# Kernel tuning notes

Measured on AMD Instinct MI355X. Metric: run time of the kernel, lower is better.

## Reference

```python
import jax, jax.numpy as jnp
import numpy as np

C = 16          # cardinality (hard-coded in GraphHead)
E = 1024        # node_encoding_size == representation_size (residual requires equality)
S = 1024        # spatial_head output size (hard-coded Linear(256,1024))
R = 1024        # representation_size
D = R // C      # sub_repr_size = 64
NS, NO = 64, 256
NUM_ITER = 2
EPS = 1e-5


def _w(key, shape, fan_in):
    return jax.random.normal(key, shape, dtype=jnp.float32) * np.float32((2.0 / fan_in) ** 0.5)


def setup_inputs() -> dict:
    key = jax.random.key(0)
    ks = jax.random.split(key, 16)
    inp = {
        'h': jax.random.normal(ks[0], (NS, E), dtype=jnp.float32),
        'o': jax.random.normal(ks[1], (NO, E), dtype=jnp.float32),
        'spatial': jax.random.normal(ks[2], (NS, NO, S), dtype=jnp.float32),
        # attention_head: MultiBranchFusion(2E, 1024, R, 16)
        'att_w1': _w(ks[3], (C, 2 * E, D), 2 * E), 'att_b1': jnp.zeros((C, D), jnp.float32),
        'att_w2': _w(ks[4], (C, S, D), S),         'att_b2': jnp.zeros((C, D), jnp.float32),
        'att_w3': _w(ks[5], (C, D, R), D),         'att_b3': jnp.zeros((C, R), jnp.float32),
        # sub_to_obj: MessageMBF(E, 1024, R, 'subject', 16)
        's2o_w1': _w(ks[6], (C, E, D), E),         's2o_b1': jnp.zeros((C, D), jnp.float32),
        's2o_w2': _w(ks[7], (C, S, D), S),         's2o_b2': jnp.zeros((C, D), jnp.float32),
        's2o_w3': _w(ks[8], (C, D, R), D),         's2o_b3': jnp.zeros((C, R), jnp.float32),
        # obj_to_sub: MessageMBF(E, 1024, R, 'object', 16)
        'o2s_w1': _w(ks[9], (C, E, D), E),         'o2s_b1': jnp.zeros((C, D), jnp.float32),
        'o2s_w2': _w(ks[10], (C, S, D), S),        'o2s_b2': jnp.zeros((C, D), jnp.float32),
        'o2s_w3': _w(ks[11], (C, D, R), D),        'o2s_b3': jnp.zeros((C, R), jnp.float32),
        # adjacency: Linear(R, 1)
        'adj_w': _w(ks[12], (R, 1), R), 'adj_b': jnp.zeros((1,), jnp.float32),
        # LayerNorms
        'ns_g': jnp.ones((E,), jnp.float32), 'ns_b': jnp.zeros((E,), jnp.float32),
        'no_g': jnp.ones((E,), jnp.float32), 'no_b': jnp.zeros((E,), jnp.float32),
    }
    return inp


def _layernorm(x, g, b):
    m = jnp.mean(x, axis=-1, keepdims=True)
    v = jnp.mean((x - m) ** 2, axis=-1, keepdims=True)
    return (x - m) * jax.lax.rsqrt(v + EPS) * g + b


def _mbf_pair(app, spa, w1, b1, w2, b2, w3, b3):
    # app [ns,no,A], spa [ns,no,S] -> [ns,no,R]; sum over C branches of fc3(relu(fc1*fc2))
    a = jnp.einsum('ija,cad->cijd', app, w1) + b1[:, None, None, :]
    s = jnp.einsum('ijs,csd->cijd', spa, w2) + b2[:, None, None, :]
    g = jax.nn.relu(a * s)
    return jnp.einsum('cijd,cdr->ijr', g, w3) + b3.sum(0)


def _msg_subject(h, spa, w1, b1, w2, b2, w3, b3):
    # MessageMBF subject: broadcast fc1(h) [ns,d] against fc2(spa) [ns,no,d]
    a = jnp.einsum('ia,cad->cid', h, w1) + b1[:, None, :]
    s = jnp.einsum('ijs,csd->cijd', spa, w2) + b2[:, None, None, :]
    g = jax.nn.relu(a[:, :, None, :] * s)
    return jnp.einsum('cijd,cdr->ijr', g, w3) + b3.sum(0)  # [ns,no,R]


def _msg_object(o, spa, w1, b1, w2, b2, w3, b3):
    # MessageMBF object: broadcast fc1(o) [no,d] against fc2(spa) [ns,no,d]
    a = jnp.einsum('ja,cad->cjd', o, w1) + b1[:, None, :]
    s = jnp.einsum('ijs,csd->cijd', spa, w2) + b2[:, None, None, :]
    g = jax.nn.relu(a[:, None, :, :] * s)
    return jnp.einsum('cijd,cdr->ijr', g, w3) + b3.sum(0)  # [ns,no,R]


def reference(h, o, spatial,
              att_w1, att_b1, att_w2, att_b2, att_w3, att_b3,
              s2o_w1, s2o_b1, s2o_w2, s2o_b2, s2o_w3, s2o_b3,
              o2s_w1, o2s_b1, o2s_w2, o2s_b2, o2s_w3, o2s_b3,
              adj_w, adj_b, ns_g, ns_b, no_g, no_b):
    ns, no = h.shape[0], o.shape[0]
    for _ in range(NUM_ITER):
        # edge weights via attention MBF on concatenated pair encodings
        pair_app = jnp.concatenate([
            jnp.broadcast_to(h[:, None, :], (ns, no, E)),
            jnp.broadcast_to(o[None, :, :], (ns, no, E)),
        ], axis=-1)
        w = jax.nn.relu(_mbf_pair(pair_app, spatial, att_w1, att_b1, att_w2, att_b2, att_w3, att_b3))
        adj = jnp.einsum('ijr,rk->ij', w, adj_w) + adj_b[0]  # [ns,no]
        # update subject nodes from object messages
        m_o2s = _msg_object(o, spatial, o2s_w1, o2s_b1, o2s_w2, o2s_b2, o2s_w3, o2s_b3)
        msg_h = jax.nn.relu(jnp.einsum('ij,ijr->ir', jax.nn.softmax(adj, axis=1), m_o2s))
        h = _layernorm(h + msg_h, ns_g, ns_b)
        # update object nodes from (updated) subject messages
        m_s2o = _msg_subject(h, spatial, s2o_w1, s2o_b1, s2o_w2, s2o_b2, s2o_w3, s2o_b3)
        msg_o = jax.nn.relu(jnp.einsum('ij,ijr->jr', jax.nn.softmax(adj, axis=0), m_s2o))
        o = _layernorm(o + msg_o, no_g, no_b)
    return jnp.concatenate([h, o], axis=0)  # [ns+no, E]
```

## Files before the change

### kernel.cpp

```cpp
#include <hip/hip_runtime.h>
#include <cstdint>
#include <cstddef>

typedef _Float16 hf;
typedef _Float16 h8v __attribute__((ext_vector_type(8)));
typedef float f4v __attribute__((ext_vector_type(4)));

#define NS 64
#define NO 256
#define MP 16384
#define KD 1024

__device__ __forceinline__ h8v cvt8(float4 a, float4 b) {
    h8v r;
    r[0] = (hf)a.x; r[1] = (hf)a.y; r[2] = (hf)a.z; r[3] = (hf)a.w;
    r[4] = (hf)b.x; r[5] = (hf)b.y; r[6] = (hf)b.z; r[7] = (hf)b.w;
    return r;
}
__device__ __forceinline__ float f4at(const float4& a, const float4& b, int e) {
    const float* p = e < 4 ? (const float*)&a : (const float*)&b;
    return p[e & 3];
}
__device__ __forceinline__ void gl16(const hf* g, hf* l) {
    __builtin_amdgcn_global_load_lds(
        (const __attribute__((address_space(1))) void*)g,
        (__attribute__((address_space(3))) void*)l, 16, 0, 0);
}

__global__ void k_pack16(const float* __restrict__ src, hf* __restrict__ dst, int n8) {
    int g = blockIdx.x * 256 + threadIdx.x;
    if (g >= n8) return;
    const float4* s4 = (const float4*)src;
    float4 a = s4[2 * g], b = s4[2 * g + 1];
    *(h8v*)(dst + (size_t)g * 8) = cvt8(a, b);
}

struct RoR { const float* src; hf* dhi; hf* dlo; int Asrc; int aOff; };
struct RoRs { RoR r[7]; };
__global__ void k_reorder16b(RoRs RR) {
    const RoR rt = RR.r[blockIdx.z];
    __shared__ float tile[64][65];
    int c = blockIdx.x, a0 = blockIdx.y * 64;
    int t = threadIdx.x, lx = t & 63, ly = t >> 6;
#pragma unroll
    for (int p = 0; p < 16; ++p) {
        int ar = ly + p * 4;
        tile[ar][lx] = rt.src[(size_t)(c * rt.Asrc + rt.aOff + a0 + ar) * 64 + lx];
    }
    __syncthreads();
#pragma unroll
    for (int p = 0; p < 16; ++p) {
        int d = ly + p * 4;
        float v = tile[lx][d];
        hf h = (hf)v;
        size_t idx = (size_t)(c * 64 + d) * 1024 + a0 + lx;
        rt.dhi[idx] = h;
        if (rt.dlo) rt.dlo[idx] = (hf)(v - (float)h);
    }
}

struct TrR { const float* src; hf* dhi; hf* dlo; };
struct TrRs { TrR r[3]; };
__global__ void k_transpose16b(TrRs RR) {
    const TrR rt = RR.r[blockIdx.z];
    __shared__ float tile[64][65];
    int r0 = blockIdx.x * 64, s0 = blockIdx.y * 64;
    int t = threadIdx.x, lx = t & 63, ly = t >> 6;
#pragma unroll
    for (int p = 0; p < 16; ++p) {
        int srow = ly + p * 4;
        tile[srow][lx] = rt.src[(size_t)(s0 + srow) * 1024 + r0 + lx];
    }
    __syncthreads();
#pragma unroll
    for (int p = 0; p < 16; ++p) {
        int rr = ly + p * 4;
        float v = tile[lx][rr];
        hf h = (hf)v;
        size_t idx = (size_t)(r0 + rr) * 1024 + s0 + lx;
        rt.dhi[idx] = h;
        if (rt.dlo) rt.dlo[idx] = (hf)(v - (float)h);
    }
}

__global__ void k_prep_bc(const float* __restrict__ ab2, const float* __restrict__ ob2,
                          const float* __restrict__ sb2, const float* __restrict__ ab3,
                          const float* __restrict__ ob3, const float* __restrict__ sb3,
                          float* __restrict__ b2cat, float* __restrict__ b3a,
                          float* __restrict__ b3o, float* __restrict__ b3s) {
    int g = blockIdx.x * 256 + threadIdx.x;
    if (g >= 1024) return;
    b2cat[g] = ab2[g]; b2cat[1024 + g] = ob2[g]; b2cat[2048 + g] = sb2[g];
    float sa = 0.f, so = 0.f, ss = 0.f;
    for (int c = 0; c < 16; ++c) {
        sa += ab3[c * 1024 + g];
        so += ob3[c * 1024 + g];
        ss += sb3[c * 1024 + g];
    }
    b3a[g] = sa; b3o[g] = so; b3s[g] = ss;
}

__global__ void k_init_ho(const float* __restrict__ h, const float* __restrict__ o,
                          float* __restrict__ outbuf, hf* __restrict__ h16, hf* __restrict__ o16) {
    int g = blockIdx.x * 256 + threadIdx.x;
    if (g < NS * KD) { float v = h[g]; outbuf[g] = v; h16[g] = (hf)v; }
    int g2 = g - NS * KD;
    if (g2 >= 0 && g2 < NO * KD) { float v = o[g2]; outbuf[NS * KD + g2] = v; o16[g2] = (hf)v; }
}

__global__ __launch_bounds__(256, 2) void k_prep_gemm(
    const hf* __restrict__ sp16,
    const hf* __restrict__ Wah, const hf* __restrict__ Wal,
    const hf* __restrict__ Wo2, const hf* __restrict__ Ws2,
    const float* __restrict__ b2cat,
    hf* __restrict__ Sh, hf* __restrict__ Sl,
    hf* __restrict__ So, hf* __restrict__ Ss) {
    __shared__ hf Ah[4096];
    __shared__ hf Bh[8192];
    __shared__ hf Bl[8192];
    const int tid = threadIdx.x;
    int lin = blockIdx.y * 12 + blockIdx.x;
    int xcd = lin & 7, slot = lin >> 3;
    int xn = slot % 12;
    const int m0 = ((xcd << 4) + slot / 12) * 128;
    const int plane = xn >> 2;
    const int nbase = (xn & 3) * 256;
    const hf* Bb = plane == 0 ? Wah : (plane == 1 ? Wo2 : Ws2);
    const bool hasL = (plane == 0);
    const int lane = tid & 63, wid = tid >> 6;
    const int wm = wid >> 1, wn = wid & 1;
    const int lr = lane & 15, lg = lane >> 4;
    const int rsl = (lg ^ ((lr >> 1) & 3)) * 8;

    const int crow = lane >> 2;
    const int gseg = ((lane & 3) ^ ((lane >> 3) & 3)) * 8;
    hf* ldsA0 = Ah + wid * 512;
    hf* ldsA1 = Ah + 2048 + wid * 512;
    hf* ldsB0 = Bh + wid * 512;         hf* ldsB1 = Bh + 2048 + wid * 512;
    hf* ldsB2 = Bh + 4096 + wid * 512;  hf* ldsB3 = Bh + 6144 + wid * 512;
    hf* ldsL0 = Bl + wid * 512;         hf* ldsL1 = Bl + 2048 + wid * 512;
    hf* ldsL2 = Bl + 4096 + wid * 512;  hf* ldsL3 = Bl + 6144 + wid * 512;
    const hf* gA0 = sp16 + (size_t)(m0 + wid * 16 + crow) * KD + gseg;
    const hf* gA1 = sp16 + (size_t)(m0 + 64 + wid * 16 + crow) * KD + gseg;
    const hf* gB0 = Bb  + (size_t)(nbase +       wid * 16 + crow) * KD + gseg;
    const hf* gB1 = Bb  + (size_t)(nbase + 64  + wid * 16 + crow) * KD + gseg;
    const hf* gB2 = Bb  + (size_t)(nbase + 128 + wid * 16 + crow) * KD + gseg;
    const hf* gB3 = Bb  + (size_t)(nbase + 192 + wid * 16 + crow) * KD + gseg;
    const hf* gL0 = Wal + (size_t)(nbase +       wid * 16 + crow) * KD + gseg;
    const hf* gL1 = Wal + (size_t)(nbase + 64  + wid * 16 + crow) * KD + gseg;
    const hf* gL2 = Wal + (size_t)(nbase + 128 + wid * 16 + crow) * KD + gseg;
    const hf* gL3 = Wal + (size_t)(nbase + 192 + wid * 16 + crow) * KD + gseg;

    f4v acc[2][4][4];
    f4v zz; zz[0] = 0.f; zz[1] = 0.f; zz[2] = 0.f; zz[3] = 0.f;
#pragma unroll
    for (int u = 0; u < 2; ++u)
#pragma unroll
        for (int a = 0; a < 4; ++a)
#pragma unroll
            for (int b = 0; b < 4; ++b) acc[u][a][b] = zz;

    for (int t = 0; t < 32; ++t) {
        const int kk = t * 32;
        __syncthreads();
        gl16(gA0 + kk, ldsA0);
        gl16(gA1 + kk, ldsA1);
        gl16(gB0 + kk, ldsB0); gl16(gB1 + kk, ldsB1);
        gl16(gB2 + kk, ldsB2); gl16(gB3 + kk, ldsB3);
        if (hasL) {
            gl16(gL0 + kk, ldsL0); gl16(gL1 + kk, ldsL1);
            gl16(gL2 + kk, ldsL2); gl16(gL3 + kk, ldsL3);
        }
        __syncthreads();
        h8v fa[4], fb[4];
#pragma unroll
        for (int x = 0; x < 4; ++x)
            fa[x] = *(const h8v*)(Ah + (wm * 64 + x * 16 + lr) * 32 + rsl);
#pragma unroll
        for (int u = 0; u < 2; ++u) {
#pragma unroll
            for (int x = 0; x < 4; ++x)
                fb[x] = *(const h8v*)(Bh + u * 4096 + (wn * 64 + x * 16 + lr) * 32 + rsl);
#pragma unroll
            for (int mi = 0; mi < 4; ++mi)
#pragma unroll
                for (int ni = 0; ni < 4; ++ni)
                    acc[u][mi][ni] = __builtin_amdgcn_mfma_f32_16x16x32_f16(fa[mi], fb[ni], acc[u][mi][ni], 0, 0, 0);
            if (hasL) {
#pragma unroll
                for (int x = 0; x < 4; ++x)
                    fb[x] = *(const h8v*)(Bl + u * 4096 + (wn * 64 + x * 16 + lr) * 32 + rsl);
#pragma unroll
                for (int mi = 0; mi < 4; ++mi)
#pragma unroll
                    for (int ni = 0; ni < 4; ++ni)
                        acc[u][mi][ni] = __builtin_amdgcn_mfma_f32_16x16x32_f16(fa[mi], fb[ni], acc[u][mi][ni], 0, 0, 0);
            }
        }
    }
#pragma unroll
    for (int u = 0; u < 2; ++u)
#pragma unroll
        for (int mi = 0; mi < 4; ++mi)
#pragma unroll
            for (int ni = 0; ni < 4; ++ni)
#pragma unroll
                for (int r = 0; r < 4; ++r) {
                    int gr = m0 + wm * 64 + mi * 16 + lg * 4 + r;
                    int col = nbase + u * 128 + wn * 64 + ni * 16 + lr;
                    float v = acc[u][mi][ni][r] + b2cat[plane * 1024 + col];
                    size_t idx = (size_t)gr * KD + col;
                    if (plane == 0) {
                        hf hi = (hf)v;
                        Sh[idx] = hi; Sl[idx] = (hf)(v - (float)hi);
                    } else if (plane == 1) So[idx] = (hf)v;
                    else Ss[idx] = (hf)v;
                }
}

__global__ void k_build_g(const hf* __restrict__ Sh, const hf* __restrict__ Sl,
                          const float* __restrict__ e1, const float* __restrict__ e2,
                          hf* __restrict__ Gh) {
    int g = blockIdx.x * 256 + threadIdx.x;
    size_t base = (size_t)g * 8;
    int m = (int)(base >> 10);
    int k = (int)(base & 1023);
    int i = m >> 8, j = m & 255;
    h8v sh = *(const h8v*)(Sh + base);
    h8v sl = *(const h8v*)(Sl + base);
    float4 ex0 = *(const float4*)(e1 + (size_t)i * KD + k);
    float4 ex1 = *(const float4*)(e1 + (size_t)i * KD + k + 4);
    float4 ey0 = *(const float4*)(e2 + (size_t)j * KD + k);
    float4 ey1 = *(const float4*)(e2 + (size_t)j * KD + k + 4);
    h8v gh;
#pragma unroll
    for (int e = 0; e < 8; ++e) {
        float s = (float)sh[e] + (float)sl[e];
        float ee = f4at(ex0, ex1, e) + f4at(ey0, ey1, e);
        float gg = ee * s; gg = gg > 0.f ? gg : 0.f;
        gh[e] = (hf)gg;
    }
    *(h8v*)(Gh + base) = gh;
}

__global__ __launch_bounds__(256, 2) void k_adj_gemm(
    const hf* __restrict__ Gh, const hf* __restrict__ W3h, const hf* __restrict__ W3l,
    const float* __restrict__ b3, const float* __restrict__ aw,
    float* __restrict__ adjv) {
    __shared__ hf Ah[4096];
    __shared__ hf Bh[8192];
    __shared__ hf Bl[8192];
    const int tid = threadIdx.x;
    int lin = blockIdx.y * 4 + blockIdx.x;
    int xcd = lin & 7, slot = lin >> 3;
    const int nbase = (slot & 3) * 256;
    const int m0 = ((xcd << 4) + (slot >> 2)) * 128;
    const int lane = tid & 63, wid = tid >> 6;
    const int wm = wid >> 1, wn = wid & 1;
    const int lr = lane & 15, lg = lane >> 4;
    const int srow = tid >> 2, sseg = tid & 3;
    const int wo_ = srow * 32 + (sseg ^ ((srow >> 1) & 3)) * 8;
    const int rsl = (lg ^ ((lr >> 1) & 3)) * 8;
    const int ar0 = m0 + srow, ar1 = ar0 + 64;
    const int ko = sseg * 8;

    f4v acc[2][4][4];
    f4v zz; zz[0] = 0.f; zz[1] = 0.f; zz[2] = 0.f; zz[3] = 0.f;
#pragma unroll
    for (int u = 0; u < 2; ++u)
#pragma unroll
        for (int a = 0; a < 4; ++a)
#pragma unroll
            for (int b = 0; b < 4; ++b) acc[u][a][b] = zz;

    h8v va0, va1, vb00, vb01, vb10, vb11, wb00, wb01, wb10, wb11;
    auto LOAD = [&](int kk) {
        va0 = *(const h8v*)(Gh + (size_t)ar0 * KD + ko + kk);
        va1 = *(const h8v*)(Gh + (size_t)ar1 * KD + ko + kk);
        vb00 = *(const h8v*)(W3h + (size_t)(nbase + srow) * KD + ko + kk);
        vb01 = *(const h8v*)(W3h + (size_t)(nbase + 64 + srow) * KD + ko + kk);
        vb10 = *(const h8v*)(W3h + (size_t)(nbase + 128 + srow) * KD + ko + kk);
        vb11 = *(const h8v*)(W3h + (size_t)(nbase + 192 + srow) * KD + ko + kk);
        wb00 = *(const h8v*)(W3l + (size_t)(nbase + srow) * KD + ko + kk);
        wb01 = *(const h8v*)(W3l + (size_t)(nbase + 64 + srow) * KD + ko + kk);
        wb10 = *(const h8v*)(W3l + (size_t)(nbase + 128 + srow) * KD + ko + kk);
        wb11 = *(const h8v*)(W3l + (size_t)(nbase + 192 + srow) * KD + ko + kk);
    };
    LOAD(0);
    for (int t = 0; t < 32; ++t) {
        __syncthreads();
        *(h8v*)(Ah + wo_) = va0; *(h8v*)(Ah + 2048 + wo_) = va1;
        *(h8v*)(Bh + wo_) = vb00; *(h8v*)(Bh + 2048 + wo_) = vb01;
        *(h8v*)(Bh + 4096 + wo_) = vb10; *(h8v*)(Bh + 6144 + wo_) = vb11;
        *(h8v*)(Bl + wo_) = wb00; *(h8v*)(Bl + 2048 + wo_) = wb01;
        *(h8v*)(Bl + 4096 + wo_) = wb10; *(h8v*)(Bl + 6144 + wo_) = wb11;
        __syncthreads();
        if (t + 1 < 32) LOAD((t + 1) * 32);
        h8v fa[4], fb[4];
#pragma unroll
        for (int x = 0; x < 4; ++x)
            fa[x] = *(const h8v*)(Ah + (wm * 64 + x * 16 + lr) * 32 + rsl);
#pragma unroll
        for (int u = 0; u < 2; ++u) {
#pragma unroll
            for (int x = 0; x < 4; ++x)
                fb[x] = *(const h8v*)(Bh + u * 4096 + (wn * 64 + x * 16 + lr) * 32 + rsl);
#pragma unroll
            for (int mi = 0; mi < 4; ++mi)
#pragma unroll
                for (int ni = 0; ni < 4; ++ni)
                    acc[u][mi][ni] = __builtin_amdgcn_mfma_f32_16x16x32_f16(fa[mi], fb[ni], acc[u][mi][ni], 0, 0, 0);
#pragma unroll
            for (int x = 0; x < 4; ++x)
                fb[x] = *(const h8v*)(Bl + u * 4096 + (wn * 64 + x * 16 + lr) * 32 + rsl);
#pragma unroll
            for (int mi = 0; mi < 4; ++mi)
#pragma unroll
                for (int ni = 0; ni < 4; ++ni)
                    acc[u][mi][ni] = __builtin_amdgcn_mfma_f32_16x16x32_f16(fa[mi], fb[ni], acc[u][mi][ni], 0, 0, 0);
        }
    }
    float b3v[2][4], awv[2][4];
#pragma unroll
    for (int u = 0; u < 2; ++u)
#pragma unroll
        for (int ni = 0; ni < 4; ++ni) {
            int gc = nbase + u * 128 + wn * 64 + ni * 16 + lr;
            b3v[u][ni] = b3[gc]; awv[u][ni] = aw[gc];
        }
#pragma unroll
    for (int mi = 0; mi < 4; ++mi)
#pragma unroll
        for (int r = 0; r < 4; ++r) {
            float part = 0.f;
#pragma unroll
            for (int u = 0; u < 2; ++u)
#pragma unroll
                for (int ni = 0; ni < 4; ++ni) {
                    float w = acc[u][mi][ni][r] + b3v[u][ni];
                    w = w > 0.f ? w : 0.f;
                    part += w * awv[u][ni];
                }
            part += __shfl_xor(part, 1);
            part += __shfl_xor(part, 2);
            part += __shfl_xor(part, 4);
            part += __shfl_xor(part, 8);
            if (lr == 0) atomicAdd(adjv + m0 + wm * 64 + mi * 16 + lg * 4 + r, part);
        }
}

struct SRoute { const hf* A; const hf* Bh; const hf* Bl; float* C; const float* bias; int m0; int M; };
struct SRoutes { SRoute r[5]; };

__global__ __launch_bounds__(256) void k_small(SRoutes RR) {
    const SRoute rt = RR.r[blockIdx.y];
    __shared__ hf Ah[4096];
    __shared__ hf Bh[4096];
    __shared__ hf Bl[4096];
    const int tid = threadIdx.x;
    const int n0 = blockIdx.x * 128;
    const int kbeg = blockIdx.z * 128;
    const int lane = tid & 63, wid = tid >> 6;
    const int wm = wid >> 1, wn = wid & 1;
    const int lr = lane & 15, lg = lane >> 4;
    const int srow = tid >> 2, sseg = tid & 3;
    const int wo_ = srow * 32 + (sseg ^ ((srow >> 1) & 3)) * 8;
    const int rsl = (lg ^ ((lr >> 1) & 3)) * 8;
    int ar0 = rt.m0 + srow;      if (ar0 >= rt.M) ar0 = rt.M - 1;
    int ar1 = rt.m0 + 64 + srow; if (ar1 >= rt.M) ar1 = rt.M - 1;
    const bool hasL = rt.Bl != nullptr;
    const int ko = kbeg + sseg * 8;

    f4v acc[4][4];
    f4v zz; zz[0] = 0.f; zz[1] = 0.f; zz[2] = 0.f; zz[3] = 0.f;
#pragma unroll
    for (int a = 0; a < 4; ++a)
#pragma unroll
        for (int b = 0; b < 4; ++b) acc[a][b] = zz;

    h8v va0, va1, vb0, vb1, wb0, wb1;
    auto LOAD = [&](int kk) {
        va0 = *(const h8v*)(rt.A + (size_t)ar0 * KD + ko + kk);
        va1 = *(const h8v*)(rt.A + (size_t)ar1 * KD + ko + kk);
        vb0 = *(const h8v*)(rt.Bh + (size_t)(n0 + srow) * KD + ko + kk);
        vb1 = *(const h8v*)(rt.Bh + (size_t)(n0 + 64 + srow) * KD + ko + kk);
        if (hasL) {
            wb0 = *(const h8v*)(rt.Bl + (size_t)(n0 + srow) * KD + ko + kk);
            wb1 = *(const h8v*)(rt.Bl + (size_t)(n0 + 64 + srow) * KD + ko + kk);
        }
    };
    LOAD(0);
    for (int t = 0; t < 4; ++t) {
        __syncthreads();
        *(h8v*)(Ah + wo_) = va0; *(h8v*)(Ah + 2048 + wo_) = va1;
        *(h8v*)(Bh + wo_) = vb0; *(h8v*)(Bh + 2048 + wo_) = vb1;
        if (hasL) { *(h8v*)(Bl + wo_) = wb0; *(h8v*)(Bl + 2048 + wo_) = wb1; }
        __syncthreads();
        if (t + 1 < 4) LOAD((t + 1) * 32);
        h8v fa[4], fb[4];
#pragma unroll
        for (int x = 0; x < 4; ++x) {
            fa[x] = *(const h8v*)(Ah + (wm * 64 + x * 16 + lr) * 32 + rsl);
            fb[x] = *(const h8v*)(Bh + (wn * 64 + x * 16 + lr) * 32 + rsl);
        }
#pragma unroll
        for (int mi = 0; mi < 4; ++mi)
#pragma unroll
            for (int ni = 0; ni < 4; ++ni)
                acc[mi][ni] = __builtin_amdgcn_mfma_f32_16x16x32_f16(fa[mi], fb[ni], acc[mi][ni], 0, 0, 0);
        if (hasL) {
#pragma unroll
            for (int x = 0; x < 4; ++x)
                fb[x] = *(const h8v*)(Bl + (wn * 64 + x * 16 + lr) * 32 + rsl);
#pragma unroll
            for (int mi = 0; mi < 4; ++mi)
#pragma unroll
                for (int ni = 0; ni < 4; ++ni)
                    acc[mi][ni] = __builtin_amdgcn_mfma_f32_16x16x32_f16(fa[mi], fb[ni], acc[mi][ni], 0, 0, 0);
        }
    }
#pragma unroll
    for (int mi = 0; mi < 4; ++mi)
#pragma unroll
        for (int ni = 0; ni < 4; ++ni)
#pragma unroll
            for (int r = 0; r < 4; ++r) {
                int gr = rt.m0 + wm * 64 + mi * 16 + lg * 4 + r;
                int gc = n0 + wn * 64 + ni * 16 + lr;
                if (gr < rt.M) {
                    float v = acc[mi][ni][r];
                    if (rt.bias && blockIdx.z == 0) v += rt.bias[gc];
                    atomicAdd(rt.C + (size_t)gr * KD + gc, v);
                }
            }
}

__global__ void k_softmax_both(const float* __restrict__ adj, float* __restrict__ p,
                               float* __restrict__ q) {
    int b = blockIdx.x;
    if (b < NS) {
        __shared__ float red[256];
        int i = b, j = threadIdx.x;
        float x = adj[i * 256 + j];
        red[j] = x; __syncthreads();
        for (int s = 128; s > 0; s >>= 1) { if (j < s) red[j] = fmaxf(red[j], red[j + s]); __syncthreads(); }
        float mx = red[0]; __syncthreads();
        float e = __expf(x - mx);
        red[j] = e; __syncthreads();
        for (int s = 128; s > 0; s >>= 1) { if (j < s) red[j] += red[j + s]; __syncthreads(); }
        p[i * 256 + j] = e / red[0];
    } else {
        int j = (b - NS) * 4 + (threadIdx.x >> 6);
        int i = threadIdx.x & 63;
        float x = adj[i * 256 + j];
        float mx = x;
#pragma unroll
        for (int off = 32; off > 0; off >>= 1) mx = fmaxf(mx, __shfl_xor(mx, off));
        float e = __expf(x - mx);
        float s = e;
#pragma unroll
        for (int off = 32; off > 0; off >>= 1) s += __shfl_xor(s, off);
        q[i * 256 + j] = e / s;
    }
}

__global__ void k_build_Gh(const hf* __restrict__ S, const float* __restrict__ aF,
                           const float* __restrict__ p, hf* __restrict__ Gh) {
    __shared__ float pl[256];
    int i = blockIdx.x;
    int k = blockIdx.y * 256 + threadIdx.x;
    pl[threadIdx.x] = p[i * 256 + threadIdx.x];
    __syncthreads();
    const hf* sp = S + (size_t)(i * 256) * KD + k;
    float acc = 0.f;
#pragma unroll 4
    for (int j = 0; j < 256; ++j) {
        float a = aF[(size_t)j * KD + k];
        float s = (float)sp[(size_t)j * KD];
        float g = a * s; g = g > 0.f ? g : 0.f;
        acc += pl[j] * g;
    }
    Gh[(size_t)i * KD + k] = (hf)acc;
}

__global__ void k_build_Go(const hf* __restrict__ S, const float* __restrict__ aF,
                           const float* __restrict__ q, hf* __restrict__ Go) {
    __shared__ float ql[64];
    int j = blockIdx.x;
    int k = blockIdx.y * 256 + threadIdx.x;
    if (threadIdx.x < 64) ql[threadIdx.x] = q[threadIdx.x * 256 + j];
    __syncthreads();
    const hf* sp = S + (size_t)j * KD + k;
    float acc = 0.f;
#pragma unroll 4
    for (int i = 0; i < 64; ++i) {
        float a = aF[(size_t)i * KD + k];
        float s = (float)sp[(size_t)(i * 256) * KD];
        float g = a * s; g = g > 0.f ? g : 0.f;
        acc += ql[i] * g;
    }
    Go[(size_t)j * KD + k] = (hf)acc;
}

__global__ void k_ln_update(float* __restrict__ x, const float* __restrict__ msg,
                            const float* __restrict__ b3, const float* __restrict__ gamma,
                            const float* __restrict__ beta, hf* __restrict__ x16) {
    __shared__ float red[256];
    int r = blockIdx.x, t = threadIdx.x;
    float v[4];
    float s = 0.f;
#pragma unroll
    for (int e = 0; e < 4; ++e) {
        int idx = t + e * 256;
        float mm = msg[(size_t)r * KD + idx] + b3[idx];
        mm = mm > 0.f ? mm : 0.f;
        v[e] = x[(size_t)r * KD + idx] + mm;
        s += v[e];
    }
    red[t] = s; __syncthreads();
    for (int st = 128; st > 0; st >>= 1) { if (t < st) red[t] += red[t + st]; __syncthreads(); }
    float mean = red[0] * (1.f / 1024.f);
    __syncthreads();
    float s2 = 0.f;
#pragma unroll
    for (int e = 0; e < 4; ++e) { float d = v[e] - mean; s2 += d * d; }
    red[t] = s2; __syncthreads();
    for (int st = 128; st > 0; st >>= 1) { if (t < st) red[t] += red[t + st]; __syncthreads(); }
    float var = red[0] * (1.f / 1024.f);
    float rstd = rsqrtf(var + 1e-5f);
#pragma unroll
    for (int e = 0; e < 4; ++e) {
        int idx = t + e * 256;
        float y = (v[e] - mean) * rstd * gamma[idx] + beta[idx];
        x[(size_t)r * KD + idx] = y;
        x16[(size_t)r * KD + idx] = (hf)y;
    }
}

extern "C" void kernel_launch(void* const* d_in, const int* in_sizes, int n_in,
                              void* d_out, int out_size, void* d_ws, size_t ws_size,
                              hipStream_t stream) {
    const float* h_in    = (const float*)d_in[0];
    const float* o_in    = (const float*)d_in[1];
    const float* spatial = (const float*)d_in[2];
    const float* att_w1  = (const float*)d_in[3];
    const float* att_b1  = (const float*)d_in[4];
    const float* att_w2  = (const float*)d_in[5];
    const float* att_b2  = (const float*)d_in[6];
    const float* att_w3  = (const float*)d_in[7];
    const float* att_b3  = (const float*)d_in[8];
    const float* s2o_w1  = (const float*)d_in[9];
    const float* s2o_b1  = (const float*)d_in[10];
    const float* s2o_w2  = (const float*)d_in[11];
    const float* s2o_b2  = (const float*)d_in[12];
    const float* s2o_w3  = (const float*)d_in[13];
    const float* s2o_b3  = (const float*)d_in[14];
    const float* o2s_w1  = (const float*)d_in[15];
    const float* o2s_b1  = (const float*)d_in[16];
    const float* o2s_w2  = (const float*)d_in[17];
    const float* o2s_b2  = (const float*)d_in[18];
    const float* o2s_w3  = (const float*)d_in[19];
    const float* o2s_b3  = (const float*)d_in[20];
    const float* adj_w   = (const float*)d_in[21];
    const float* ns_g    = (const float*)d_in[23];
    const float* ns_b    = (const float*)d_in[24];
    const float* no_g    = (const float*)d_in[25];
    const float* no_b    = (const float*)d_in[26];

    char* ws = (char*)d_ws;
    size_t off = 0;
    auto alloc = [&](size_t bytes) -> char* {
        char* pp = ws + off;
        off += (bytes + 255) & ~(size_t)255;
        return pp;
    };
    const size_t PLANE = (size_t)MP * KD * sizeof(hf);
    const size_t WMAT  = (size_t)1024 * 1024 * sizeof(hf);
    hf* S_att_h = (hf*)alloc(PLANE);
    hf* S_att_l = (hf*)alloc(PLANE);
    hf* S_o2s   = (hf*)alloc(PLANE);
    hf* S_s2o   = (hf*)alloc(PLANE);
    hf* gA_h    = (hf*)alloc(PLANE);
    hf* sp16    = gA_h;
    hf* W2att_h = (hf*)alloc(WMAT); hf* W2att_l = (hf*)alloc(WMAT);
    hf* W2o2s   = (hf*)alloc(WMAT);
    hf* W2s2o   = (hf*)alloc(WMAT);
    hf* W1ah_h  = (hf*)alloc(WMAT); hf* W1ah_l  = (hf*)alloc(WMAT);
    hf* W1ao_h  = (hf*)alloc(WMAT); hf* W1ao_l  = (hf*)alloc(WMAT);
    hf* W1o2s   = (hf*)alloc(WMAT);
    hf* W1s2o   = (hf*)alloc(WMAT);
    hf* W3a_h   = (hf*)alloc(WMAT); hf* W3a_l   = (hf*)alloc(WMAT);
    hf* W3o     = (hf*)alloc(WMAT);
    hf* W3s     = (hf*)alloc(WMAT);
    float* b2cat = (float*)alloc(3072 * 4);
    float* b3a   = (float*)alloc(1024 * 4);
    float* b3o   = (float*)alloc(1024 * 4);
    float* b3s   = (float*)alloc(1024 * 4);
    float* fc1h = (float*)alloc((size_t)NS * KD * 4);
    float* fc1o = (float*)alloc((size_t)NO * KD * 4);
    float* aO2S = (float*)alloc((size_t)NO * KD * 4);
    float* aS2O = (float*)alloc((size_t)NS * KD * 4);
    float* msgh = (float*)alloc((size_t)NS * KD * 4);
    float* msgo = (float*)alloc((size_t)NO * KD * 4);
    float* adjv = (float*)alloc((size_t)MP * 4);
    char* zend_ = (char*)(adjv + MP);
    size_t zlen = (size_t)(zend_ - (char*)fc1h);
    float* pbuf = (float*)alloc((size_t)MP * 4);
    float* qbuf = (float*)alloc((size_t)MP * 4);
    hf* h16 = (hf*)alloc((size_t)NS * KD * sizeof(hf));
    hf* o16 = (hf*)alloc((size_t)NO * KD * sizeof(hf));
    hf* Gh  = (hf*)alloc((size_t)NS * KD * sizeof(hf));
    hf* Go  = (hf*)alloc((size_t)NO * KD * sizeof(hf));

    float* hbuf = (float*)d_out;
    float* obuf = (float*)d_out + NS * KD;

    k_pack16<<<dim3(MP * KD / 8 / 256), 256, 0, stream>>>(spatial, sp16, MP * KD / 8);
    {
        RoRs R;
        R.r[0] = { att_w2, W2att_h, W2att_l, 1024, 0 };
        R.r[1] = { o2s_w2, W2o2s, nullptr, 1024, 0 };
        R.r[2] = { s2o_w2, W2s2o, nullptr, 1024, 0 };
        R.r[3] = { att_w1, W1ah_h, W1ah_l, 2048, 0 };
        R.r[4] = { att_w1, W1ao_h, W1ao_l, 2048, 1024 };
        R.r[5] = { o2s_w1, W1o2s, nullptr, 1024, 0 };
        R.r[6] = { s2o_w1, W1s2o, nullptr, 1024, 0 };
        k_reorder16b<<<dim3(16, 16, 7), 256, 0, stream>>>(R);
    }
    {
        TrRs T;
        T.r[0] = { att_w3, W3a_h, W3a_l };
        T.r[1] = { o2s_w3, W3o, nullptr };
        T.r[2] = { s2o_w3, W3s, nullptr };
        k_transpose16b<<<dim3(16, 16, 3), 256, 0, stream>>>(T);
    }
    k_prep_bc<<<dim3(4), 256, 0, stream>>>(att_b2, o2s_b2, s2o_b2, att_b3, o2s_b3, s2o_b3,
                                           b2cat, b3a, b3o, b3s);
    k_init_ho<<<dim3(1280), 256, 0, stream>>>(h_in, o_in, (float*)d_out, h16, o16);
    k_prep_gemm<<<dim3(12, 128), 256, 0, stream>>>(sp16, W2att_h, W2att_l, W2o2s, W2s2o,
                                                   b2cat, S_att_h, S_att_l, S_o2s, S_s2o);

    for (int it = 0; it < 2; ++it) {
        hipMemsetAsync(fc1h, 0, zlen, stream);
        {
            SRoutes R;
            R.r[0] = { h16, W1ah_h, W1ah_l, fc1h, att_b1, 0,   NS };
            R.r[1] = { o16, W1ao_h, W1ao_l, fc1o, nullptr, 0,   NO };
            R.r[2] = { o16, W1ao_h, W1ao_l, fc1o, nullptr, 128, NO };
            R.r[3] = { o16, W1o2s,  nullptr, aO2S, o2s_b1, 0,   NO };
            R.r[4] = { o16, W1o2s,  nullptr, aO2S, o2s_b1, 128, NO };
            k_small<<<dim3(8, 5, 8), 256, 0, stream>>>(R);
        }
        k_build_g<<<dim3(MP * KD / 8 / 256), 256, 0, stream>>>(S_att_h, S_att_l, fc1h, fc1o, gA_h);
        k_adj_gemm<<<dim3(4, 128), 256, 0, stream>>>(gA_h, W3a_h, W3a_l, b3a, adj_w, adjv);
        k_softmax_both<<<dim3(NS + NO / 4), 256, 0, stream>>>(adjv, pbuf, qbuf);
        k_build_Gh<<<dim3(NS, 4), 256, 0, stream>>>(S_o2s, aO2S, pbuf, Gh);
        {
            SRoutes R;
            R.r[0] = { Gh, W3o, nullptr, msgh, nullptr, 0, NS };
            k_small<<<dim3(8, 1, 8), 256, 0, stream>>>(R);
        }
        k_ln_update<<<dim3(NS), 256, 0, stream>>>(hbuf, msgh, b3o, ns_g, ns_b, h16);
        {
            SRoutes R;
            R.r[0] = { h16, W1s2o, nullptr, aS2O, s2o_b1, 0, NS };
            k_small<<<dim3(8, 1, 8), 256, 0, stream>>>(R);
        }
        k_build_Go<<<dim3(NO, 4), 256, 0, stream>>>(S_s2o, aS2O, qbuf, Go);
        {
            SRoutes R;
            R.r[0] = { Go, W3s, nullptr, msgo, nullptr, 0,   NO };
            R.r[1] = { Go, W3s, nullptr, msgo, nullptr, 128, NO };
            k_small<<<dim3(8, 2, 8), 256, 0, stream>>>(R);
        }
        k_ln_update<<<dim3(NO), 256, 0, stream>>>(obuf, msgo, b3s, no_g, no_b, o16);
    }
    (void)in_sizes; (void)n_in; (void)out_size; (void)ws_size;
}
```

Measured before the change: 620.8 us.

## Double-buffer LDS tiles with async global-to-LDS loads in both GEMM kernels

```diff
diff --git a/kernel.cpp b/kernel.cpp
--- a/kernel.cpp
+++ b/kernel.cpp
@@ -115,9 +115,9 @@
     const float* __restrict__ b2cat,
     hf* __restrict__ Sh, hf* __restrict__ Sl,
     hf* __restrict__ So, hf* __restrict__ Ss) {
-    __shared__ hf Ah[4096];
-    __shared__ hf Bh[8192];
-    __shared__ hf Bl[8192];
+    __shared__ hf Ah[2][4096];
+    __shared__ hf Bh[2][8192];
+    __shared__ hf Bl[2][8192];
     const int tid = threadIdx.x;
     int lin = blockIdx.y * 12 + blockIdx.x;
     int xcd = lin & 7, slot = lin >> 3;
@@ -134,12 +134,7 @@
 
     const int crow = lane >> 2;
     const int gseg = ((lane & 3) ^ ((lane >> 3) & 3)) * 8;
-    hf* ldsA0 = Ah + wid * 512;
-    hf* ldsA1 = Ah + 2048 + wid * 512;
-    hf* ldsB0 = Bh + wid * 512;         hf* ldsB1 = Bh + 2048 + wid * 512;
-    hf* ldsB2 = Bh + 4096 + wid * 512;  hf* ldsB3 = Bh + 6144 + wid * 512;
-    hf* ldsL0 = Bl + wid * 512;         hf* ldsL1 = Bl + 2048 + wid * 512;
-    hf* ldsL2 = Bl + 4096 + wid * 512;  hf* ldsL3 = Bl + 6144 + wid * 512;
+    const int aoff = wid * 512;
     const hf* gA0 = sp16 + (size_t)(m0 + wid * 16 + crow) * KD + gseg;
     const hf* gA1 = sp16 + (size_t)(m0 + 64 + wid * 16 + crow) * KD + gseg;
     const hf* gB0 = Bb  + (size_t)(nbase +       wid * 16 + crow) * KD + gseg;
@@ -151,6 +146,17 @@
     const hf* gL2 = Wal + (size_t)(nbase + 128 + wid * 16 + crow) * KD + gseg;
     const hf* gL3 = Wal + (size_t)(nbase + 192 + wid * 16 + crow) * KD + gseg;
 
+    auto STAGE = [&](int b, int kk) {
+        gl16(gA0 + kk, Ah[b] + aoff);
+        gl16(gA1 + kk, Ah[b] + 2048 + aoff);
+        gl16(gB0 + kk, Bh[b] + aoff);        gl16(gB1 + kk, Bh[b] + 2048 + aoff);
+        gl16(gB2 + kk, Bh[b] + 4096 + aoff); gl16(gB3 + kk, Bh[b] + 6144 + aoff);
+        if (hasL) {
+            gl16(gL0 + kk, Bl[b] + aoff);        gl16(gL1 + kk, Bl[b] + 2048 + aoff);
+            gl16(gL2 + kk, Bl[b] + 4096 + aoff); gl16(gL3 + kk, Bl[b] + 6144 + aoff);
+        }
+    };
+
     f4v acc[2][4][4];
     f4v zz; zz[0] = 0.f; zz[1] = 0.f; zz[2] = 0.f; zz[3] = 0.f;
 #pragma unroll
@@ -160,27 +166,21 @@
 #pragma unroll
             for (int b = 0; b < 4; ++b) acc[u][a][b] = zz;
 
+    STAGE(0, 0);
+    __syncthreads();
+    int cur = 0;
     for (int t = 0; t < 32; ++t) {
-        const int kk = t * 32;
-        __syncthreads();
-        gl16(gA0 + kk, ldsA0);
-        gl16(gA1 + kk, ldsA1);
-        gl16(gB0 + kk, ldsB0); gl16(gB1 + kk, ldsB1);
-        gl16(gB2 + kk, ldsB2); gl16(gB3 + kk, ldsB3);
-        if (hasL) {
-            gl16(gL0 + kk, ldsL0); gl16(gL1 + kk, ldsL1);
-            gl16(gL2 + kk, ldsL2); gl16(gL3 + kk, ldsL3);
-        }
-        __syncthreads();
+        if (t + 1 < 32) STAGE(cur ^ 1, (t + 1) * 32);
+        const hf* A = Ah[cur]; const hf* B = Bh[cur]; const hf* BL = Bl[cur];
         h8v fa[4], fb[4];
 #pragma unroll
         for (int x = 0; x < 4; ++x)
-            fa[x] = *(const h8v*)(Ah + (wm * 64 + x * 16 + lr) * 32 + rsl);
+            fa[x] = *(const h8v*)(A + (wm * 64 + x * 16 + lr) * 32 + rsl);
 #pragma unroll
         for (int u = 0; u < 2; ++u) {
 #pragma unroll
             for (int x = 0; x < 4; ++x)
-                fb[x] = *(const h8v*)(Bh + u * 4096 + (wn * 64 + x * 16 + lr) * 32 + rsl);
+                fb[x] = *(const h8v*)(B + u * 4096 + (wn * 64 + x * 16 + lr) * 32 + rsl);
 #pragma unroll
             for (int mi = 0; mi < 4; ++mi)
 #pragma unroll
@@ -189,7 +189,7 @@
             if (hasL) {
 #pragma unroll
                 for (int x = 0; x < 4; ++x)
-                    fb[x] = *(const h8v*)(Bl + u * 4096 + (wn * 64 + x * 16 + lr) * 32 + rsl);
+                    fb[x] = *(const h8v*)(BL + u * 4096 + (wn * 64 + x * 16 + lr) * 32 + rsl);
 #pragma unroll
                 for (int mi = 0; mi < 4; ++mi)
 #pragma unroll
@@ -197,6 +197,8 @@
                         acc[u][mi][ni] = __builtin_amdgcn_mfma_f32_16x16x32_f16(fa[mi], fb[ni], acc[u][mi][ni], 0, 0, 0);
             }
         }
+        __syncthreads();
+        cur ^= 1;
     }
 #pragma unroll
     for (int u = 0; u < 2; ++u)
@@ -206,7 +208,7 @@
             for (int ni = 0; ni < 4; ++ni)
 #pragma unroll
                 for (int r = 0; r < 4; ++r) {
-                    int gr = m0 + wm * 64 + mi * 16 + lg * 4 + r;
+                    int gr = m0 + wm * 64 + mi * 16 + (lane >> 4) * 4 + r;
                     int col = nbase + u * 128 + wn * 64 + ni * 16 + lr;
                     float v = acc[u][mi][ni][r] + b2cat[plane * 1024 + col];
                     size_t idx = (size_t)gr * KD + col;
@@ -247,9 +249,9 @@
     const hf* __restrict__ Gh, const hf* __restrict__ W3h, const hf* __restrict__ W3l,
     const float* __restrict__ b3, const float* __restrict__ aw,
     float* __restrict__ adjv) {
-    __shared__ hf Ah[4096];
-    __shared__ hf Bh[8192];
-    __shared__ hf Bl[8192];
+    __shared__ hf Ah[2][4096];
+    __shared__ hf Bh[2][8192];
+    __shared__ hf Bl[2][8192];
     const int tid = threadIdx.x;
     int lin = blockIdx.y * 4 + blockIdx.x;
     int xcd = lin & 7, slot = lin >> 3;
@@ -258,11 +260,30 @@
     const int lane = tid & 63, wid = tid >> 6;
     const int wm = wid >> 1, wn = wid & 1;
     const int lr = lane & 15, lg = lane >> 4;
-    const int srow = tid >> 2, sseg = tid & 3;
-    const int wo_ = srow * 32 + (sseg ^ ((srow >> 1) & 3)) * 8;
     const int rsl = (lg ^ ((lr >> 1) & 3)) * 8;
-    const int ar0 = m0 + srow, ar1 = ar0 + 64;
-    const int ko = sseg * 8;
+
+    const int crow = lane >> 2;
+    const int gseg = ((lane & 3) ^ ((lane >> 3) & 3)) * 8;
+    const int aoff = wid * 512;
+    const hf* gA0 = Gh  + (size_t)(m0 +       wid * 16 + crow) * KD + gseg;
+    const hf* gA1 = Gh  + (size_t)(m0 + 64 +  wid * 16 + crow) * KD + gseg;
+    const hf* gB0 = W3h + (size_t)(nbase +       wid * 16 + crow) * KD + gseg;
+    const hf* gB1 = W3h + (size_t)(nbase + 64  + wid * 16 + crow) * KD + gseg;
+    const hf* gB2 = W3h + (size_t)(nbase + 128 + wid * 16 + crow) * KD + gseg;
+    const hf* gB3 = W3h + (size_t)(nbase + 192 + wid * 16 + crow) * KD + gseg;
+    const hf* gL0 = W3l + (size_t)(nbase +       wid * 16 + crow) * KD + gseg;
+    const hf* gL1 = W3l + (size_t)(nbase + 64  + wid * 16 + crow) * KD + gseg;
+    const hf* gL2 = W3l + (size_t)(nbase + 128 + wid * 16 + crow) * KD + gseg;
+    const hf* gL3 = W3l + (size_t)(nbase + 192 + wid * 16 + crow) * KD + gseg;
+
+    auto STAGE = [&](int b, int kk) {
+        gl16(gA0 + kk, Ah[b] + aoff);
+        gl16(gA1 + kk, Ah[b] + 2048 + aoff);
+        gl16(gB0 + kk, Bh[b] + aoff);        gl16(gB1 + kk, Bh[b] + 2048 + aoff);
+        gl16(gB2 + kk, Bh[b] + 4096 + aoff); gl16(gB3 + kk, Bh[b] + 6144 + aoff);
+        gl16(gL0 + kk, Bl[b] + aoff);        gl16(gL1 + kk, Bl[b] + 2048 + aoff);
+        gl16(gL2 + kk, Bl[b] + 4096 + aoff); gl16(gL3 + kk, Bl[b] + 6144 + aoff);
+    };
 
     f4v acc[2][4][4];
     f4v zz; zz[0] = 0.f; zz[1] = 0.f; zz[2] = 0.f; zz[3] = 0.f;
@@ -273,38 +294,21 @@
 #pragma unroll
             for (int b = 0; b < 4; ++b) acc[u][a][b] = zz;
 
-    h8v va0, va1, vb00, vb01, vb10, vb11, wb00, wb01, wb10, wb11;
-    auto LOAD = [&](int kk) {
-        va0 = *(const h8v*)(Gh + (size_t)ar0 * KD + ko + kk);
-        va1 = *(const h8v*)(Gh + (size_t)ar1 * KD + ko + kk);
-        vb00 = *(const h8v*)(W3h + (size_t)(nbase + srow) * KD + ko + kk);
-        vb01 = *(const h8v*)(W3h + (size_t)(nbase + 64 + srow) * KD + ko + kk);
-        vb10 = *(const h8v*)(W3h + (size_t)(nbase + 128 + srow) * KD + ko + kk);
-        vb11 = *(const h8v*)(W3h + (size_t)(nbase + 192 + srow) * KD + ko + kk);
-        wb00 = *(const h8v*)(W3l + (size_t)(nbase + srow) * KD + ko + kk);
-        wb01 = *(const h8v*)(W3l + (size_t)(nbase + 64 + srow) * KD + ko + kk);
-        wb10 = *(const h8v*)(W3l + (size_t)(nbase + 128 + srow) * KD + ko + kk);
-        wb11 = *(const h8v*)(W3l + (size_t)(nbase + 192 + srow) * KD + ko + kk);
-    };
-    LOAD(0);
+    STAGE(0, 0);
+    __syncthreads();
+    int cur = 0;
     for (int t = 0; t < 32; ++t) {
-        __syncthreads();
-        *(h8v*)(Ah + wo_) = va0; *(h8v*)(Ah + 2048 + wo_) = va1;
-        *(h8v*)(Bh + wo_) = vb00; *(h8v*)(Bh + 2048 + wo_) = vb01;
-        *(h8v*)(Bh + 4096 + wo_) = vb10; *(h8v*)(Bh + 6144 + wo_) = vb11;
-        *(h8v*)(Bl + wo_) = wb00; *(h8v*)(Bl + 2048 + wo_) = wb01;
-        *(h8v*)(Bl + 4096 + wo_) = wb10; *(h8v*)(Bl + 6144 + wo_) = wb11;
-        __syncthreads();
-        if (t + 1 < 32) LOAD((t + 1) * 32);
+        if (t + 1 < 32) STAGE(cur ^ 1, (t + 1) * 32);
+        const hf* A = Ah[cur]; const hf* B = Bh[cur]; const hf* BL = Bl[cur];
         h8v fa[4], fb[4];
 #pragma unroll
         for (int x = 0; x < 4; ++x)
-            fa[x] = *(const h8v*)(Ah + (wm * 64 + x * 16 + lr) * 32 + rsl);
+            fa[x] = *(const h8v*)(A + (wm * 64 + x * 16 + lr) * 32 + rsl);
 #pragma unroll
         for (int u = 0; u < 2; ++u) {
 #pragma unroll
             for (int x = 0; x < 4; ++x)
-                fb[x] = *(const h8v*)(Bh + u * 4096 + (wn * 64 + x * 16 + lr) * 32 + rsl);
+                fb[x] = *(const h8v*)(B + u * 4096 + (wn * 64 + x * 16 + lr) * 32 + rsl);
 #pragma unroll
             for (int mi = 0; mi < 4; ++mi)
 #pragma unroll
@@ -312,13 +316,15 @@
                     acc[u][mi][ni] = __builtin_amdgcn_mfma_f32_16x16x32_f16(fa[mi], fb[ni], acc[u][mi][ni], 0, 0, 0);
 #pragma unroll
             for (int x = 0; x < 4; ++x)
-                fb[x] = *(const h8v*)(Bl + u * 4096 + (wn * 64 + x * 16 + lr) * 32 + rsl);
+                fb[x] = *(const h8v*)(BL + u * 4096 + (wn * 64 + x * 16 + lr) * 32 + rsl);
 #pragma unroll
             for (int mi = 0; mi < 4; ++mi)
 #pragma unroll
                 for (int ni = 0; ni < 4; ++ni)
                     acc[u][mi][ni] = __builtin_amdgcn_mfma_f32_16x16x32_f16(fa[mi], fb[ni], acc[u][mi][ni], 0, 0, 0);
         }
+        __syncthreads();
+        cur ^= 1;
     }
     float b3v[2][4], awv[2][4];
 #pragma unroll
```

After: 624.5 us. About the same (+0.6%).

## Fuse gated pair-activation build into adjacency GEMM A-tile loading

Applied to the files above, without the earlier changes.

```diff
diff --git a/kernel.cpp b/kernel.cpp
--- a/kernel.cpp
+++ b/kernel.cpp
@@ -218,33 +218,10 @@
                 }
 }
 
-__global__ void k_build_g(const hf* __restrict__ Sh, const hf* __restrict__ Sl,
-                          const float* __restrict__ e1, const float* __restrict__ e2,
-                          hf* __restrict__ Gh) {
-    int g = blockIdx.x * 256 + threadIdx.x;
-    size_t base = (size_t)g * 8;
-    int m = (int)(base >> 10);
-    int k = (int)(base & 1023);
-    int i = m >> 8, j = m & 255;
-    h8v sh = *(const h8v*)(Sh + base);
-    h8v sl = *(const h8v*)(Sl + base);
-    float4 ex0 = *(const float4*)(e1 + (size_t)i * KD + k);
-    float4 ex1 = *(const float4*)(e1 + (size_t)i * KD + k + 4);
-    float4 ey0 = *(const float4*)(e2 + (size_t)j * KD + k);
-    float4 ey1 = *(const float4*)(e2 + (size_t)j * KD + k + 4);
-    h8v gh;
-#pragma unroll
-    for (int e = 0; e < 8; ++e) {
-        float s = (float)sh[e] + (float)sl[e];
-        float ee = f4at(ex0, ex1, e) + f4at(ey0, ey1, e);
-        float gg = ee * s; gg = gg > 0.f ? gg : 0.f;
-        gh[e] = (hf)gg;
-    }
-    *(h8v*)(Gh + base) = gh;
-}
-
 __global__ __launch_bounds__(256, 2) void k_adj_gemm(
-    const hf* __restrict__ Gh, const hf* __restrict__ W3h, const hf* __restrict__ W3l,
+    const hf* __restrict__ Sh, const hf* __restrict__ Sl,
+    const float* __restrict__ e1, const float* __restrict__ e2,
+    const hf* __restrict__ W3h, const hf* __restrict__ W3l,
     const float* __restrict__ b3, const float* __restrict__ aw,
     float* __restrict__ adjv) {
     __shared__ hf Ah[4096];
@@ -262,6 +239,8 @@
     const int wo_ = srow * 32 + (sseg ^ ((srow >> 1) & 3)) * 8;
     const int rsl = (lg ^ ((lr >> 1) & 3)) * 8;
     const int ar0 = m0 + srow, ar1 = ar0 + 64;
+    const int i0 = ar0 >> 8, j0 = ar0 & 255;
+    const int i1 = ar1 >> 8, j1 = ar1 & 255;
     const int ko = sseg * 8;
 
     f4v acc[2][4][4];
@@ -273,10 +252,23 @@
 #pragma unroll
             for (int b = 0; b < 4; ++b) acc[u][a][b] = zz;
 
-    h8v va0, va1, vb00, vb01, vb10, vb11, wb00, wb01, wb10, wb11;
+    h8v sh0, sl0, sh1, sl1;
+    float4 ex00, ex01, ey00, ey01, ex10, ex11, ey10, ey11;
+    h8v vb00, vb01, vb10, vb11, wb00, wb01, wb10, wb11;
+    h8v gh0, gh1;
     auto LOAD = [&](int kk) {
-        va0 = *(const h8v*)(Gh + (size_t)ar0 * KD + ko + kk);
-        va1 = *(const h8v*)(Gh + (size_t)ar1 * KD + ko + kk);
+        sh0 = *(const h8v*)(Sh + (size_t)ar0 * KD + ko + kk);
+        sl0 = *(const h8v*)(Sl + (size_t)ar0 * KD + ko + kk);
+        sh1 = *(const h8v*)(Sh + (size_t)ar1 * KD + ko + kk);
+        sl1 = *(const h8v*)(Sl + (size_t)ar1 * KD + ko + kk);
+        ex00 = *(const float4*)(e1 + (size_t)i0 * KD + ko + kk);
+        ex01 = *(const float4*)(e1 + (size_t)i0 * KD + ko + kk + 4);
+        ey00 = *(const float4*)(e2 + (size_t)j0 * KD + ko + kk);
+        ey01 = *(const float4*)(e2 + (size_t)j0 * KD + ko + kk + 4);
+        ex10 = *(const float4*)(e1 + (size_t)i1 * KD + ko + kk);
+        ex11 = *(const float4*)(e1 + (size_t)i1 * KD + ko + kk + 4);
+        ey10 = *(const float4*)(e2 + (size_t)j1 * KD + ko + kk);
+        ey11 = *(const float4*)(e2 + (size_t)j1 * KD + ko + kk + 4);
         vb00 = *(const h8v*)(W3h + (size_t)(nbase + srow) * KD + ko + kk);
         vb01 = *(const h8v*)(W3h + (size_t)(nbase + 64 + srow) * KD + ko + kk);
         vb10 = *(const h8v*)(W3h + (size_t)(nbase + 128 + srow) * KD + ko + kk);
@@ -286,16 +278,33 @@
         wb10 = *(const h8v*)(W3l + (size_t)(nbase + 128 + srow) * KD + ko + kk);
         wb11 = *(const h8v*)(W3l + (size_t)(nbase + 192 + srow) * KD + ko + kk);
     };
+    auto BUILD = [&]() {
+#pragma unroll
+        for (int e = 0; e < 8; ++e) {
+            float s = (float)sh0[e] + (float)sl0[e];
+            float ee = f4at(ex00, ex01, e) + f4at(ey00, ey01, e);
+            float gg = ee * s; gg = gg > 0.f ? gg : 0.f;
+            gh0[e] = (hf)gg;
+        }
+#pragma unroll
+        for (int e = 0; e < 8; ++e) {
+            float s = (float)sh1[e] + (float)sl1[e];
+            float ee = f4at(ex10, ex11, e) + f4at(ey10, ey11, e);
+            float gg = ee * s; gg = gg > 0.f ? gg : 0.f;
+            gh1[e] = (hf)gg;
+        }
+    };
     LOAD(0);
+    BUILD();
     for (int t = 0; t < 32; ++t) {
         __syncthreads();
-        *(h8v*)(Ah + wo_) = va0; *(h8v*)(Ah + 2048 + wo_) = va1;
+        *(h8v*)(Ah + wo_) = gh0; *(h8v*)(Ah + 2048 + wo_) = gh1;
         *(h8v*)(Bh + wo_) = vb00; *(h8v*)(Bh + 2048 + wo_) = vb01;
         *(h8v*)(Bh + 4096 + wo_) = vb10; *(h8v*)(Bh + 6144 + wo_) = vb11;
         *(h8v*)(Bl + wo_) = wb00; *(h8v*)(Bl + 2048 + wo_) = wb01;
         *(h8v*)(Bl + 4096 + wo_) = wb10; *(h8v*)(Bl + 6144 + wo_) = wb11;
         __syncthreads();
-        if (t + 1 < 32) LOAD((t + 1) * 32);
+        if (t + 1 < 32) { LOAD((t + 1) * 32); BUILD(); }
         h8v fa[4], fb[4];
 #pragma unroll
         for (int x = 0; x < 4; ++x)
@@ -580,8 +589,7 @@
     hf* S_att_l = (hf*)alloc(PLANE);
     hf* S_o2s   = (hf*)alloc(PLANE);
     hf* S_s2o   = (hf*)alloc(PLANE);
-    hf* gA_h    = (hf*)alloc(PLANE);
-    hf* sp16    = gA_h;
+    hf* sp16    = (hf*)alloc(PLANE);
     hf* W2att_h = (hf*)alloc(WMAT); hf* W2att_l = (hf*)alloc(WMAT);
     hf* W2o2s   = (hf*)alloc(WMAT);
     hf* W2s2o   = (hf*)alloc(WMAT);
@@ -651,8 +659,8 @@
             R.r[4] = { o16, W1o2s,  nullptr, aO2S, o2s_b1, 128, NO };
             k_small<<<dim3(8, 5, 8), 256, 0, stream>>>(R);
         }
-        k_build_g<<<dim3(MP * KD / 8 / 256), 256, 0, stream>>>(S_att_h, S_att_l, fc1h, fc1o, gA_h);
-        k_adj_gemm<<<dim3(4, 128), 256, 0, stream>>>(gA_h, W3a_h, W3a_l, b3a, adj_w, adjv);
+        k_adj_gemm<<<dim3(4, 128), 256, 0, stream>>>(S_att_h, S_att_l, fc1h, fc1o,
+                                                     W3a_h, W3a_l, b3a, adj_w, adjv);
         k_softmax_both<<<dim3(NS + NO / 4), 256, 0, stream>>>(adjv, pbuf, qbuf);
         k_build_Gh<<<dim3(NS, 4), 256, 0, stream>>>(S_o2s, aO2S, pbuf, Gh);
         {
```

Measured after the change: 617.0 us. Within noise of the previous version (-0.6%).
